# Kernel tuning notes

Measured on AMD Instinct MI355X. Metric: run time of the kernel, lower is better.

## Reference

```python
import jax, jax.numpy as jnp
import numpy as np

N_NODES = 100000
N_EDGES = 1250000
D_FEAT = 64


def setup_inputs() -> dict:
    key = jax.random.key(0)
    k1, k2, k3 = jax.random.split(key, 3)
    index = jax.random.randint(k1, (N_EDGES,), 0, N_NODES, dtype=jnp.int64)
    A = jax.random.normal(k2, (N_NODES, D_FEAT), dtype=jnp.float32)
    B = jax.random.normal(k3, (N_EDGES, D_FEAT), dtype=jnp.float32)
    return {"index": index, "A": A, "B": B}


def reference(index, A, B):
    # The torch module's unique/index_put/python-loop chain is semantically a
    # single scatter-add: A[index[i]] += B[i] for all i, with accumulation
    # over duplicate indices.
    return A.at[index].add(B)
```

## Files before the change

kernel.cpp:

```cpp
#include <hip/hip_runtime.h>


#define D_FEAT    64
#define ROW_INTS  64
#define CAP_SLOTS 63

__global__ void scatter_add_kernel(const int* __restrict__ index,
                                   const float* __restrict__ B,
                                   float* __restrict__ out,
                                   long long total) {
    long long i = (long long)blockIdx.x * blockDim.x + threadIdx.x;
    if (i >= total) return;
    int e = (int)(i >> 6);
    int f = (int)(i & 63);
    int node = index[e];
    atomicAdd(&out[(long long)node * D_FEAT + f], B[i]);
}

__global__ void zero_kernel(int* __restrict__ rows, int* __restrict__ ovf_cnt,
                            int n_nodes) {
    int i = blockIdx.x * blockDim.x + threadIdx.x;
    if (i < n_nodes) rows[(long long)i * ROW_INTS] = 0;
    if (i == 0) *ovf_cnt = 0;
}

__device__ __forceinline__ void place_one(int v, int eid,
                                          int* __restrict__ rows,
                                          int* __restrict__ ovf_cnt,
                                          int* __restrict__ ovf,
                                          int ovf_capacity) {
    int* row = rows + (long long)v * ROW_INTS;
    int pos = atomicAdd(row, 1);
    if (pos < CAP_SLOTS) {
        row[1 + pos] = eid;
    } else {
        int op = atomicAdd(ovf_cnt, 1);
        if (op < ovf_capacity) ovf[op] = eid;
    }
}

__global__ void place_kernel(const int* __restrict__ index,
                             int* __restrict__ rows,
                             int* __restrict__ ovf_cnt,
                             int* __restrict__ ovf,
                             int ovf_capacity,
                             int n) {
    int i = (blockIdx.x * blockDim.x + threadIdx.x) * 4;
    if (i + 3 < n) {
        int4 v = *(const int4*)(index + i);
        place_one(v.x, i + 0, rows, ovf_cnt, ovf, ovf_capacity);
        place_one(v.y, i + 1, rows, ovf_cnt, ovf, ovf_capacity);
        place_one(v.z, i + 2, rows, ovf_cnt, ovf, ovf_capacity);
        place_one(v.w, i + 3, rows, ovf_cnt, ovf, ovf_capacity);
    } else {
        for (int k = i; k < n; ++k)
            place_one(index[k], k, rows, ovf_cnt, ovf, ovf_capacity);
    }
}

__global__ __launch_bounds__(256) void gather_kernel(
    const int* __restrict__ rows,
    const float* __restrict__ A,
    const float* __restrict__ B,
    float* __restrict__ out, int n_nodes)
{
    int wave = (int)((blockIdx.x * (long long)blockDim.x + threadIdx.x) >> 6);
    int lane = threadIdx.x & 63;
    if (wave >= n_nodes) return;

    int rowval = rows[(long long)wave * ROW_INTS + lane];
    int c = __shfl(rowval, 0, 64);
    if (c > CAP_SLOTS) c = CAP_SLOTS;

    long long oidx = (long long)wave * D_FEAT + lane;
    float acc = A[oidx];

    int j = 0;
    for (; j + 7 < c; j += 8) {
        int e0 = __shfl(rowval, 1 + j + 0, 64);
        int e1 = __shfl(rowval, 1 + j + 1, 64);
        int e2 = __shfl(rowval, 1 + j + 2, 64);
        int e3 = __shfl(rowval, 1 + j + 3, 64);
        int e4 = __shfl(rowval, 1 + j + 4, 64);
        int e5 = __shfl(rowval, 1 + j + 5, 64);
        int e6 = __shfl(rowval, 1 + j + 6, 64);
        int e7 = __shfl(rowval, 1 + j + 7, 64);
        float b0 = B[(long long)e0 * D_FEAT + lane];
        float b1 = B[(long long)e1 * D_FEAT + lane];
        float b2 = B[(long long)e2 * D_FEAT + lane];
        float b3 = B[(long long)e3 * D_FEAT + lane];
        float b4 = B[(long long)e4 * D_FEAT + lane];
        float b5 = B[(long long)e5 * D_FEAT + lane];
        float b6 = B[(long long)e6 * D_FEAT + lane];
        float b7 = B[(long long)e7 * D_FEAT + lane];
        acc += b0; acc += b1; acc += b2; acc += b3;
        acc += b4; acc += b5; acc += b6; acc += b7;
    }
    for (; j + 3 < c; j += 4) {
        int e0 = __shfl(rowval, 1 + j + 0, 64);
        int e1 = __shfl(rowval, 1 + j + 1, 64);
        int e2 = __shfl(rowval, 1 + j + 2, 64);
        int e3 = __shfl(rowval, 1 + j + 3, 64);
        float b0 = B[(long long)e0 * D_FEAT + lane];
        float b1 = B[(long long)e1 * D_FEAT + lane];
        float b2 = B[(long long)e2 * D_FEAT + lane];
        float b3 = B[(long long)e3 * D_FEAT + lane];
        acc += b0; acc += b1; acc += b2; acc += b3;
    }
    for (; j < c; ++j) {
        int e0 = __shfl(rowval, 1 + j, 64);
        acc += B[(long long)e0 * D_FEAT + lane];
    }
    out[oidx] = acc;
}

__global__ void cleanup_kernel(const int* __restrict__ ovf_cnt,
                               const int* __restrict__ ovf,
                               const int* __restrict__ index,
                               const float* __restrict__ B,
                               float* __restrict__ out,
                               int ovf_capacity) {
    int n = *ovf_cnt;
    if (n > ovf_capacity) n = ovf_capacity;
    int nwaves = (gridDim.x * blockDim.x) >> 6;
    int wid = (int)((blockIdx.x * (long long)blockDim.x + threadIdx.x) >> 6);
    int lane = threadIdx.x & 63;
    for (int i = wid; i < n; i += nwaves) {
        int eid = __builtin_amdgcn_readfirstlane(ovf[i]);
        int node = __builtin_amdgcn_readfirstlane(index[eid]);
        atomicAdd(&out[(long long)node * D_FEAT + lane],
                  B[(long long)eid * D_FEAT + lane]);
    }
}

extern "C" void kernel_launch(void* const* d_in, const int* in_sizes, int n_in,
                              void* d_out, int out_size, void* d_ws, size_t ws_size,
                              hipStream_t stream) {
    const int*   index = (const int*)d_in[0];
    const float* A     = (const float*)d_in[1];
    const float* B     = (const float*)d_in[2];
    float*       out   = (float*)d_out;

    const int n_edges = in_sizes[0];
    const int n_nodes = out_size / D_FEAT;

    size_t need = (1
                   + (size_t)n_edges
                   + (size_t)n_nodes * ROW_INTS
                  ) * sizeof(int);

    if (ws_size < need) {
        hipMemcpyAsync(out, A, (size_t)out_size * sizeof(float),
                       hipMemcpyDeviceToDevice, stream);
        long long total = (long long)n_edges * D_FEAT;
        int block = 256;
        long long grid = (total + block - 1) / block;
        scatter_add_kernel<<<(int)grid, block, 0, stream>>>(index, B, out, total);
        return;
    }

    int* ovf_cnt = (int*)d_ws;
    int* ovf     = ovf_cnt + 1;
    int* rows    = ovf + n_edges;
    rows = (int*)(((uintptr_t)rows + 255) & ~(uintptr_t)255);

    const int block = 256;

    zero_kernel<<<(n_nodes + block - 1) / block, block, 0, stream>>>(
        rows, ovf_cnt, n_nodes);
    {
        int nthreads = (n_edges + 3) / 4;
        place_kernel<<<(nthreads + block - 1) / block, block, 0, stream>>>(
            index, rows, ovf_cnt, ovf, n_edges, n_edges);
    }
    {
        long long threads = (long long)n_nodes * 64;
        int grid = (int)((threads + block - 1) / block);
        gather_kernel<<<grid, block, 0, stream>>>(rows, A, B, out, n_nodes);
    }
    cleanup_kernel<<<512, block, 0, stream>>>(ovf_cnt, ovf, index, B, out, n_edges);
}
```

Baseline: 142.6 us.

## Vectorize gather with float4 lane groups and fold overflow into gather

The gather kernel now splits each wave into four 16-lane groups that each load a whole B row as float4, processing four edges per iteration, and combines the partial sums with xor shuffles. The separate cleanup kernel is removed. Overflow entries now store (edge, node) pairs and every wave linearly scans the overflow list to add its own matches. This cuts per-edge load instruction count and one launch, but the overflow scan is O(n_overflow) per node, which costs little only while the overflow list stays near empty, as it should with about 12 edges per node against 63 slots.

```diff
diff --git a/kernel.cpp b/kernel.cpp
--- a/kernel.cpp
+++ b/kernel.cpp
@@ -27,7 +27,7 @@
 __device__ __forceinline__ void place_one(int v, int eid,
                                           int* __restrict__ rows,
                                           int* __restrict__ ovf_cnt,
-                                          int* __restrict__ ovf,
+                                          int2* __restrict__ ovf,
                                           int ovf_capacity) {
     int* row = rows + (long long)v * ROW_INTS;
     int pos = atomicAdd(row, 1);
@@ -35,14 +35,14 @@
         row[1 + pos] = eid;
     } else {
         int op = atomicAdd(ovf_cnt, 1);
-        if (op < ovf_capacity) ovf[op] = eid;
+        if (op < ovf_capacity) ovf[op] = make_int2(eid, v);
     }
 }
 
 __global__ void place_kernel(const int* __restrict__ index,
                              int* __restrict__ rows,
                              int* __restrict__ ovf_cnt,
-                             int* __restrict__ ovf,
+                             int2* __restrict__ ovf,
                              int ovf_capacity,
                              int n) {
     int i = (blockIdx.x * blockDim.x + threadIdx.x) * 4;
@@ -60,76 +60,67 @@
 
 __global__ __launch_bounds__(256) void gather_kernel(
     const int* __restrict__ rows,
+    const int* __restrict__ ovf_cnt,
+    const int2* __restrict__ ovf,
     const float* __restrict__ A,
     const float* __restrict__ B,
-    float* __restrict__ out, int n_nodes)
+    float* __restrict__ out, int n_nodes, int ovf_capacity)
 {
     int wave = (int)((blockIdx.x * (long long)blockDim.x + threadIdx.x) >> 6);
     int lane = threadIdx.x & 63;
     if (wave >= n_nodes) return;
+    int g   = lane >> 4;
+    int sub = lane & 15;
 
     int rowval = rows[(long long)wave * ROW_INTS + lane];
     int c = __shfl(rowval, 0, 64);
     if (c > CAP_SLOTS) c = CAP_SLOTS;
 
-    long long oidx = (long long)wave * D_FEAT + lane;
-    float acc = A[oidx];
+    float4 acc = make_float4(0.f, 0.f, 0.f, 0.f);
 
     int j = 0;
     for (; j + 7 < c; j += 8) {
-        int e0 = __shfl(rowval, 1 + j + 0, 64);
-        int e1 = __shfl(rowval, 1 + j + 1, 64);
-        int e2 = __shfl(rowval, 1 + j + 2, 64);
-        int e3 = __shfl(rowval, 1 + j + 3, 64);
-        int e4 = __shfl(rowval, 1 + j + 4, 64);
-        int e5 = __shfl(rowval, 1 + j + 5, 64);
-        int e6 = __shfl(rowval, 1 + j + 6, 64);
-        int e7 = __shfl(rowval, 1 + j + 7, 64);
-        float b0 = B[(long long)e0 * D_FEAT + lane];
-        float b1 = B[(long long)e1 * D_FEAT + lane];
-        float b2 = B[(long long)e2 * D_FEAT + lane];
-        float b3 = B[(long long)e3 * D_FEAT + lane];
-        float b4 = B[(long long)e4 * D_FEAT + lane];
-        float b5 = B[(long long)e5 * D_FEAT + lane];
-        float b6 = B[(long long)e6 * D_FEAT + lane];
-        float b7 = B[(long long)e7 * D_FEAT + lane];
-        acc += b0; acc += b1; acc += b2; acc += b3;
-        acc += b4; acc += b5; acc += b6; acc += b7;
+        int ea = __shfl(rowval, 1 + j + g, 64);
+        int eb = __shfl(rowval, 5 + j + g, 64);
+        float4 ba = *((const float4*)(B + (long long)ea * D_FEAT) + sub);
+        float4 bb = *((const float4*)(B + (long long)eb * D_FEAT) + sub);
+        acc.x += ba.x; acc.y += ba.y; acc.z += ba.z; acc.w += ba.w;
+        acc.x += bb.x; acc.y += bb.y; acc.z += bb.z; acc.w += bb.w;
     }
     for (; j + 3 < c; j += 4) {
-        int e0 = __shfl(rowval, 1 + j + 0, 64);
-        int e1 = __shfl(rowval, 1 + j + 1, 64);
-        int e2 = __shfl(rowval, 1 + j + 2, 64);
-        int e3 = __shfl(rowval, 1 + j + 3, 64);
-        float b0 = B[(long long)e0 * D_FEAT + lane];
-        float b1 = B[(long long)e1 * D_FEAT + lane];
-        float b2 = B[(long long)e2 * D_FEAT + lane];
-        float b3 = B[(long long)e3 * D_FEAT + lane];
-        acc += b0; acc += b1; acc += b2; acc += b3;
+        int ea = __shfl(rowval, 1 + j + g, 64);
+        float4 ba = *((const float4*)(B + (long long)ea * D_FEAT) + sub);
+        acc.x += ba.x; acc.y += ba.y; acc.z += ba.z; acc.w += ba.w;
     }
-    for (; j < c; ++j) {
-        int e0 = __shfl(rowval, 1 + j, 64);
-        acc += B[(long long)e0 * D_FEAT + lane];
+    {
+        int rem = c - j;
+        int src = 1 + j + g; if (src > 63) src = 63;
+        int er = __shfl(rowval, src, 64);
+        if (g < rem) {
+            float4 br = *((const float4*)(B + (long long)er * D_FEAT) + sub);
+            acc.x += br.x; acc.y += br.y; acc.z += br.z; acc.w += br.w;
+        }
     }
-    out[oidx] = acc;
-}
 
-__global__ void cleanup_kernel(const int* __restrict__ ovf_cnt,
-                               const int* __restrict__ ovf,
-                               const int* __restrict__ index,
-                               const float* __restrict__ B,
-                               float* __restrict__ out,
-                               int ovf_capacity) {
-    int n = *ovf_cnt;
-    if (n > ovf_capacity) n = ovf_capacity;
-    int nwaves = (gridDim.x * blockDim.x) >> 6;
-    int wid = (int)((blockIdx.x * (long long)blockDim.x + threadIdx.x) >> 6);
-    int lane = threadIdx.x & 63;
-    for (int i = wid; i < n; i += nwaves) {
-        int eid = __builtin_amdgcn_readfirstlane(ovf[i]);
-        int node = __builtin_amdgcn_readfirstlane(index[eid]);
-        atomicAdd(&out[(long long)node * D_FEAT + lane],
-                  B[(long long)eid * D_FEAT + lane]);
+    acc.x += __shfl_xor(acc.x, 16); acc.y += __shfl_xor(acc.y, 16);
+    acc.z += __shfl_xor(acc.z, 16); acc.w += __shfl_xor(acc.w, 16);
+    acc.x += __shfl_xor(acc.x, 32); acc.y += __shfl_xor(acc.y, 32);
+    acc.z += __shfl_xor(acc.z, 32); acc.w += __shfl_xor(acc.w, 32);
+
+    int novf = *ovf_cnt;
+    if (novf > ovf_capacity) novf = ovf_capacity;
+    for (int i = 0; i < novf; ++i) {
+        int2 p = ovf[i];
+        if (p.y == wave && g == 0) {
+            float4 br = *((const float4*)(B + (long long)p.x * D_FEAT) + sub);
+            acc.x += br.x; acc.y += br.y; acc.z += br.z; acc.w += br.w;
+        }
+    }
+
+    if (g == 0) {
+        float4 a = *((const float4*)(A + (long long)wave * D_FEAT) + sub);
+        *((float4*)(out + (long long)wave * D_FEAT) + sub) =
+            make_float4(a.x + acc.x, a.y + acc.y, a.z + acc.z, a.w + acc.w);
     }
 }
 
@@ -144,9 +135,10 @@
     const int n_edges = in_sizes[0];
     const int n_nodes = out_size / D_FEAT;
 
-    size_t need = (1
-                   + (size_t)n_edges
+    size_t need = (2
+                   + (size_t)n_edges * 2
                    + (size_t)n_nodes * ROW_INTS
+                   + 64
                   ) * sizeof(int);
 
     if (ws_size < need) {
@@ -159,9 +151,9 @@
         return;
     }
 
-    int* ovf_cnt = (int*)d_ws;
-    int* ovf     = ovf_cnt + 1;
-    int* rows    = ovf + n_edges;
+    int*  ovf_cnt = (int*)d_ws;
+    int2* ovf     = (int2*)(ovf_cnt + 2);
+    int*  rows    = (int*)(ovf + n_edges);
     rows = (int*)(((uintptr_t)rows + 255) & ~(uintptr_t)255);
 
     const int block = 256;
@@ -176,7 +168,7 @@
     {
         long long threads = (long long)n_nodes * 64;
         int grid = (int)((threads + block - 1) / block);
-        gather_kernel<<<grid, block, 0, stream>>>(rows, A, B, out, n_nodes);
+        gather_kernel<<<grid, block, 0, stream>>>(
+            rows, ovf_cnt, ovf, A, B, out, n_nodes, n_edges);
     }
-    cleanup_kernel<<<512, block, 0, stream>>>(ovf_cnt, ovf, index, B, out, n_edges);
 }
```

After: 142.8 us. Within noise of the previous version (+0.1%).
